# Kernel tuning notes

Measured on AMD Instinct MI355X. Metric: run time of the kernel, lower is better.

Reference implementation:

```python
import jax, jax.numpy as jnp
import numpy as np

B, H, W = 8, 56, 56
DIM, DIM_OUT, NUM_HEADS = 96, 192, 3
Q_STRIDE = (2, 2)


def setup_inputs() -> dict:
    key = jax.random.key(0)
    k1, k2, k3 = jax.random.split(key, 3)
    x = jax.random.normal(k1, (B, H, W, DIM), dtype=jnp.float32)
    W_qkv = jax.random.normal(k2, (DIM, 3 * DIM_OUT), dtype=jnp.float32) * 0.02
    b_qkv = jnp.zeros((3 * DIM_OUT,), dtype=jnp.float32)
    W_proj = jax.random.normal(k3, (DIM_OUT, DIM_OUT), dtype=jnp.float32) * 0.02
    b_proj = jnp.zeros((DIM_OUT,), dtype=jnp.float32)
    return {"x": x, "W_qkv": W_qkv, "b_qkv": b_qkv, "W_proj": W_proj, "b_proj": b_proj}


def reference(x, W_qkv, b_qkv, W_proj, b_proj):
    b, h, w, _ = x.shape
    c = W_proj.shape[0]          # dim_out
    nh = NUM_HEADS
    hd = c // nh                 # head_dim
    sh, sw = Q_STRIDE

    # fused QKV projection: (B,H,W,3*C)
    qkv = jnp.einsum("bhwd,de->bhwe", x, W_qkv) + b_qkv
    qkv = qkv.reshape(b, h * w, 3, nh, hd)
    q, k, v = qkv[:, :, 0], qkv[:, :, 1], qkv[:, :, 2]  # each (B,N,nh,hd)

    # query max-pool over spatial dims (channels = nh*hd, heads interleaved as in original)
    q = q.reshape(b, h, w, c)
    q = q.reshape(b, h // sh, sh, w // sw, sw, c).max(axis=(2, 4))  # (B,H',W',C)
    hn, wn = h // sh, w // sw
    q = q.reshape(b, hn * wn, nh, hd)

    # heads-first layout, scaled q
    q = q.transpose(0, 2, 1, 3) / jnp.sqrt(jnp.asarray(hd, x.dtype))  # (B,nh,Nq,hd)
    k = k.transpose(0, 2, 1, 3)                                       # (B,nh,Nk,hd)
    v = v.transpose(0, 2, 1, 3)

    attn = jax.nn.softmax(jnp.einsum("bnqd,bnkd->bnqk", q, k), axis=-1)
    out = jnp.einsum("bnqk,bnkd->bnqd", attn, v)        # (B,nh,Nq,hd)
    out = out.transpose(0, 2, 1, 3).reshape(b, hn, wn, c)

    return jnp.einsum("bhwc,cd->bhwd", out, W_proj) + b_proj
```

## Files before the change

kernel.cpp:

```cpp
#include <hip/hip_runtime.h>

#define BB    8
#define DIMO  192
#define NH    3
#define HD    64
#define NK    3136
#define NQ    784
#define M1    25088
#define M2    6272
#define KSPLIT 7
#define KSLICE 448
#define PSTR  56

#if __has_builtin(__builtin_amdgcn_mfma_f32_16x16x16bf16_1k)
#define HAVE_MFMA16 1
#else
#define HAVE_MFMA16 0
#endif

typedef __bf16 bf16x8 __attribute__((ext_vector_type(8)));
typedef float f32x4  __attribute__((ext_vector_type(4)));
typedef short s16x4  __attribute__((ext_vector_type(4)));

__device__ inline unsigned short f2bf(float f) {
    unsigned int u = __builtin_bit_cast(unsigned int, f);
    u += 0x7FFFu + ((u >> 16) & 1u);
    return (unsigned short)(u >> 16);
}

__global__ void wprep(const float* __restrict__ Wqkv, const float* __restrict__ Wproj,
                      unsigned short* __restrict__ Wb, unsigned short* __restrict__ Wpb) {
    __shared__ float Ls[192][33];
    const int t = threadIdx.x;
    if (blockIdx.x < 18) {
        const int n0 = blockIdx.x * 32;
        int rr = t >> 5, c = t & 31;
#pragma unroll
        for (int rb = 0; rb < 12; ++rb) {
            int row = rb * 8 + rr;
            Ls[row][c] = Wqkv[(size_t)row * 576 + n0 + c];
        }
        __syncthreads();
        int n = t >> 3, kc = (t & 7) * 12;
#pragma unroll
        for (int j = 0; j < 12; j += 4) {
            ushort4 u = { f2bf(Ls[kc + j][n]), f2bf(Ls[kc + j + 1][n]),
                          f2bf(Ls[kc + j + 2][n]), f2bf(Ls[kc + j + 3][n]) };
            *(ushort4*)(Wb + (size_t)(n0 + n) * 96 + kc + j) = u;
        }
    } else {
        const int n0 = (blockIdx.x - 18) * 32;
        int rr = t >> 5, c = t & 31;
#pragma unroll
        for (int rb = 0; rb < 24; ++rb) {
            int row = rb * 8 + rr;
            Ls[row][c] = Wproj[(size_t)row * 192 + n0 + c];
        }
        __syncthreads();
        int n = t >> 3, kc = (t & 7) * 24;
#pragma unroll
        for (int j = 0; j < 24; j += 4) {
            ushort4 u = { f2bf(Ls[kc + j][n]), f2bf(Ls[kc + j + 1][n]),
                          f2bf(Ls[kc + j + 2][n]), f2bf(Ls[kc + j + 3][n]) };
            *(ushort4*)(Wpb + (size_t)(n0 + n) * 192 + kc + j) = u;
        }
    }
}

__launch_bounds__(256)
__global__ void qkv_fused(const float* __restrict__ x,
                          const unsigned short* __restrict__ Wb,
                          const float* __restrict__ bias,
                          unsigned short* __restrict__ Qpb,
                          unsigned short* __restrict__ Kb,
                          unsigned short* __restrict__ Vt) {
    __shared__ __attribute__((aligned(16))) unsigned short xs[112 * 104];
    const int tid = threadIdx.x;
    const int wave = tid >> 6, lane = tid & 63;
    const int quad = lane >> 4, l16 = lane & 15;
    const int bid = blockIdx.x;

    if (bid < 784) {
        const int sec = (bid < 392) ? 1 : 2;
        const int m0 = ((bid < 392) ? bid : bid - 392) * 64;
#pragma unroll
        for (int i = 0; i < 6; ++i) {
            int f = tid + i * 256;
            int r = f / 24, c4 = f % 24;
            float4 v = ((const float4*)x)[(size_t)(m0 + r) * 24 + c4];
            ushort4 u = { f2bf(v.x), f2bf(v.y), f2bf(v.z), f2bf(v.w) };
            *(ushort4*)&xs[r * 104 + c4 * 4] = u;
        }
        __syncthreads();

        f32x4 acc[12];
#pragma unroll
        for (int i = 0; i < 12; ++i) acc[i] = (f32x4){0.f, 0.f, 0.f, 0.f};

        const unsigned short* wb = Wb + (size_t)(sec * 192 + l16) * 96 + quad * 8;
#pragma unroll
        for (int ch = 0; ch < 3; ++ch) {
            bf16x8 af = *(const bf16x8*)&xs[(wave * 16 + l16) * 104 + ch * 32 + quad * 8];
#pragma unroll
            for (int nf = 0; nf < 12; ++nf) {
                bf16x8 bfr = *(const bf16x8*)(wb + (size_t)nf * 16 * 96 + ch * 32);
                acc[nf] = __builtin_amdgcn_mfma_f32_16x16x32_bf16(af, bfr, acc[nf], 0, 0, 0);
            }
        }

        const int mbase = m0 + wave * 16 + quad * 4;
        if (sec == 1) {
#pragma unroll
            for (int nf = 0; nf < 12; ++nf) {
                int n = nf * 16 + l16;
                float bs = bias[192 + n];
#pragma unroll
                for (int i = 0; i < 4; ++i)
                    Kb[(size_t)(mbase + i) * 192 + n] = f2bf(acc[nf][i] + bs);
            }
        } else {
            int b = m0 / NK;
            int key = mbase - b * NK;
#pragma unroll
            for (int nf = 0; nf < 12; ++nf) {
                int n = nf * 16 + l16;
                float bs = bias[384 + n];
                int hh = n >> 6, dd = n & 63;
                ushort4 u = { f2bf(acc[nf][0] + bs), f2bf(acc[nf][1] + bs),
                              f2bf(acc[nf][2] + bs), f2bf(acc[nf][3] + bs) };
                *(ushort4*)(Vt + ((size_t)((b * 3 + hh) * 64 + dd)) * NK + key) = u;
            }
        }
    } else {
        const int t = bid - 784;
        const int b = t / 28, hq = t % 28;
        const int m0 = b * NK + hq * 112;
#pragma unroll
        for (int i = 0; i < 11; ++i) {
            int f = tid + i * 256;
            if (f < 2688) {
                int r = f / 24, c4 = f % 24;
                float4 v = ((const float4*)x)[(size_t)(m0 + r) * 24 + c4];
                int rp = 2 * (r % 56) + (r / 56);
                ushort4 u = { f2bf(v.x), f2bf(v.y), f2bf(v.z), f2bf(v.w) };
                *(ushort4*)&xs[rp * 104 + c4 * 4] = u;
            }
        }
        __syncthreads();

        f32x4 acc[7][3];
#pragma unroll
        for (int i = 0; i < 7; ++i)
#pragma unroll
            for (int j = 0; j < 3; ++j) acc[i][j] = (f32x4){0.f, 0.f, 0.f, 0.f};

        const unsigned short* wb = Wb + (size_t)(wave * 48 + l16) * 96 + quad * 8;
#pragma unroll
        for (int ch = 0; ch < 3; ++ch) {
            bf16x8 bfr[3];
#pragma unroll
            for (int jf = 0; jf < 3; ++jf)
                bfr[jf] = *(const bf16x8*)(wb + (size_t)jf * 16 * 96 + ch * 32);
#pragma unroll
            for (int mf = 0; mf < 7; ++mf) {
                bf16x8 a = *(const bf16x8*)&xs[(mf * 16 + l16) * 104 + ch * 32 + quad * 8];
#pragma unroll
                for (int jf = 0; jf < 3; ++jf)
                    acc[mf][jf] = __builtin_amdgcn_mfma_f32_16x16x32_bf16(a, bfr[jf], acc[mf][jf], 0, 0, 0);
            }
        }

#pragma unroll
        for (int mf = 0; mf < 7; ++mf) {
            int q = hq * 28 + mf * 4 + quad;
#pragma unroll
            for (int jf = 0; jf < 3; ++jf) {
                int n = wave * 48 + jf * 16 + l16;
                float m = fmaxf(fmaxf(acc[mf][jf][0], acc[mf][jf][1]),
                                fmaxf(acc[mf][jf][2], acc[mf][jf][3]));
                m = (m + bias[n]) * 0.125f;
                int hh = n >> 6, dd = n & 63;
                Qpb[((size_t)(b * 3 + hh) * NQ + q) * 64 + dd] = f2bf(m);
            }
        }
    }
}

__launch_bounds__(256)
__global__ void attn_mfma(const unsigned short* __restrict__ Qpb,
                          const unsigned short* __restrict__ Kb,
                          const unsigned short* __restrict__ Vt,
                          float* __restrict__ Pnum,
                          float* __restrict__ Pden) {
    __shared__ __attribute__((aligned(16))) unsigned short Ks[64 * 88];
    __shared__ __attribute__((aligned(16))) unsigned short Vs[64 * 88];
#if !HAVE_MFMA16
    __shared__ __attribute__((aligned(16))) unsigned short Ps[4 * 32 * PSTR];
#endif

    const int tid = threadIdx.x;
    const int wave = tid >> 6, lane = tid & 63;
    const int quad = lane >> 4, l16 = lane & 15;
    const int bh = blockIdx.y, b = bh / NH, h = bh % NH;
    const int qt = blockIdx.x * 128 + wave * 32;
    const int ks = blockIdx.z, k00 = ks * KSLICE;

    const int srow0 = tid >> 3, sch = (tid & 7) * 8;
    const unsigned short* kg  = Kb + ((size_t)(b * NK + k00) + srow0) * DIMO + h * 64 + sch;
    const unsigned short* kg1 = kg + (size_t)32 * DIMO;
    const unsigned short* vg  = Vt + ((size_t)bh * 64 + srow0) * NK + k00 + sch;
    const unsigned short* vg1 = vg + (size_t)32 * NK;

    uint4 kp0 = *(const uint4*)kg;
    uint4 kp1 = *(const uint4*)kg1;
    uint4 vp0 = *(const uint4*)vg;
    uint4 vp1 = *(const uint4*)vg1;

    int qa = min(qt + l16, NQ - 1);
    int qb = min(qt + 16 + l16, NQ - 1);
    const unsigned short* qpa = Qpb + ((size_t)bh * NQ + qa) * HD + quad * 8;
    const unsigned short* qpc = Qpb + ((size_t)bh * NQ + qb) * HD + quad * 8;
    bf16x8 qf[2][2];
    qf[0][0] = *(const bf16x8*)qpa;  qf[0][1] = *(const bf16x8*)(qpa + 32);
    qf[1][0] = *(const bf16x8*)qpc;  qf[1][1] = *(const bf16x8*)(qpc + 32);

    f32x4 on[4][2];
#pragma unroll
    for (int i = 0; i < 4; ++i)
#pragma unroll
        for (int j = 0; j < 2; ++j) on[i][j] = (f32x4){0.f, 0.f, 0.f, 0.f};
    float dden0 = 0.f, dden1 = 0.f;

#if !HAVE_MFMA16
    unsigned short* myP = Ps + wave * 32 * PSTR;
#endif

    for (int s = 0; s < 7; ++s) {
        __syncthreads();
        *(uint4*)&Ks[srow0 * 88 + sch]        = kp0;
        *(uint4*)&Ks[(srow0 + 32) * 88 + sch] = kp1;
        *(uint4*)&Vs[srow0 * 88 + sch]        = vp0;
        *(uint4*)&Vs[(srow0 + 32) * 88 + sch] = vp1;
        __syncthreads();
        if (s < 6) {
            kp0 = *(const uint4*)(kg  + (size_t)(s + 1) * 64 * DIMO);
            kp1 = *(const uint4*)(kg1 + (size_t)(s + 1) * 64 * DIMO);
            vp0 = *(const uint4*)(vg  + (s + 1) * 64);
            vp1 = *(const uint4*)(vg1 + (s + 1) * 64);
        }

#if HAVE_MFMA16
#pragma unroll
        for (int g = 0; g < 4; ++g) {
            const int krow = (g * 16 + l16) * 88;
            bf16x8 kf0 = *(const bf16x8*)&Ks[krow + quad * 8];
            bf16x8 kf1 = *(const bf16x8*)&Ks[krow + 32 + quad * 8];
            s16x4 vf[4];
#pragma unroll
            for (int dsub = 0; dsub < 4; ++dsub)
                vf[dsub] = *(const s16x4*)&Vs[(dsub * 16 + l16) * 88 + g * 16 + quad * 4];
#pragma unroll
            for (int qsub = 0; qsub < 2; ++qsub) {
                f32x4 sa = (f32x4){0.f, 0.f, 0.f, 0.f};
                sa = __builtin_amdgcn_mfma_f32_16x16x32_bf16(kf0, qf[qsub][0], sa, 0, 0, 0);
                sa = __builtin_amdgcn_mfma_f32_16x16x32_bf16(kf1, qf[qsub][1], sa, 0, 0, 0);
                float p0 = __expf(sa[0]), p1 = __expf(sa[1]);
                float p2 = __expf(sa[2]), p3 = __expf(sa[3]);
                if (qsub == 0) dden0 += (p0 + p1) + (p2 + p3);
                else           dden1 += (p0 + p1) + (p2 + p3);
                s16x4 pb = { (short)f2bf(p0), (short)f2bf(p1),
                             (short)f2bf(p2), (short)f2bf(p3) };
#pragma unroll
                for (int dsub = 0; dsub < 4; ++dsub)
                    on[dsub][qsub] = __builtin_amdgcn_mfma_f32_16x16x16bf16_1k(
                        vf[dsub], pb, on[dsub][qsub], 0, 0, 0);
            }
        }
#else
#pragma unroll
        for (int half = 0; half < 2; ++half) {
#pragma unroll
            for (int ksub = 0; ksub < 2; ++ksub) {
                const int krow = (half * 32 + ksub * 16 + l16) * 88;
                bf16x8 kf0 = *(const bf16x8*)&Ks[krow + quad * 8];
                bf16x8 kf1 = *(const bf16x8*)&Ks[krow + 32 + quad * 8];
#pragma unroll
                for (int qsub = 0; qsub < 2; ++qsub) {
                    f32x4 sa = (f32x4){0.f, 0.f, 0.f, 0.f};
                    sa = __builtin_amdgcn_mfma_f32_16x16x32_bf16(kf0, qf[qsub][0], sa, 0, 0, 0);
                    sa = __builtin_amdgcn_mfma_f32_16x16x32_bf16(kf1, qf[qsub][1], sa, 0, 0, 0);
                    float p0 = __expf(sa[0]), p1 = __expf(sa[1]);
                    float p2 = __expf(sa[2]), p3 = __expf(sa[3]);
                    if (qsub == 0) dden0 += (p0 + p1) + (p2 + p3);
                    else           dden1 += (p0 + p1) + (p2 + p3);
                    ushort4 pw = { f2bf(p0), f2bf(p1), f2bf(p2), f2bf(p3) };
                    *(ushort4*)&myP[(qsub * 16 + l16) * PSTR + ksub * 16 + quad * 4] = pw;
                }
            }
            bf16x8 pf0 = *(const bf16x8*)&myP[l16 * PSTR + quad * 8];
            bf16x8 pf1 = *(const bf16x8*)&myP[(16 + l16) * PSTR + quad * 8];
#pragma unroll
            for (int dsub = 0; dsub < 4; ++dsub) {
                bf16x8 vf = *(const bf16x8*)&Vs[(dsub * 16 + l16) * 88 + half * 32 + quad * 8];
                on[dsub][0] = __builtin_amdgcn_mfma_f32_16x16x32_bf16(vf, pf0, on[dsub][0], 0, 0, 0);
                on[dsub][1] = __builtin_amdgcn_mfma_f32_16x16x32_bf16(vf, pf1, on[dsub][1], 0, 0, 0);
            }
        }
#endif
    }

#pragma unroll
    for (int qsub = 0; qsub < 2; ++qsub) {
        float r = (qsub == 0) ? dden0 : dden1;
        r += __shfl_xor(r, 16, 64);
        r += __shfl_xor(r, 32, 64);
        int q = qt + qsub * 16 + l16;
        if (q < NQ) {
            size_t base = (size_t)ks * (24 * NQ * HD) + ((size_t)bh * NQ + q) * HD + quad * 4;
#pragma unroll
            for (int dsub = 0; dsub < 4; ++dsub)
                *(f32x4*)(Pnum + base + dsub * 16) = on[dsub][qsub];
            if (quad == 0) Pden[ks * (24 * NQ) + bh * NQ + q] = r;
        }
    }
}

__launch_bounds__(256)
__global__ void proj_comb(const float* __restrict__ Pnum,
                          const float* __restrict__ Pden,
                          const unsigned short* __restrict__ Wpb,
                          const float* __restrict__ bproj,
                          float* __restrict__ out) {
    __shared__ __attribute__((aligned(16))) unsigned short as_[16 * 200];
    __shared__ float rden[16][4];
    const int tid = threadIdx.x;
    const int wave = tid >> 6, lane = tid & 63;
    const int quad = lane >> 4, l16 = lane & 15;
    const int m0 = blockIdx.x * 16;

    if (tid < 48) {
        int r = tid / 3, h = tid % 3;
        int gq = m0 + r, b = gq / NQ, qq = gq - b * NQ;
        float den = 0.f;
#pragma unroll
        for (int s = 0; s < KSPLIT; ++s)
            den += Pden[s * (24 * NQ) + (b * 3 + h) * NQ + qq];
        rden[r][h] = 1.0f / den;
    }
    __syncthreads();

    {
        int r = tid >> 4, cl = tid & 15;
        int gq = m0 + r, b = gq / NQ, qq = gq - b * NQ;
#pragma unroll
        for (int i = 0; i < 3; ++i) {
            int c = cl + i * 16;
            int h = c >> 4, d = (c & 15) * 4;
            const float* p = Pnum + ((size_t)(b * 3 + h) * NQ + qq) * 64 + d;
            f32x4 num = (f32x4){0.f, 0.f, 0.f, 0.f};
#pragma unroll
            for (int s = 0; s < KSPLIT; ++s)
                num = num + *(const f32x4*)(p + (size_t)s * (24 * NQ * HD));
            float rc = rden[r][h];
            ushort4 u = { f2bf(num[0] * rc), f2bf(num[1] * rc),
                          f2bf(num[2] * rc), f2bf(num[3] * rc) };
            *(ushort4*)&as_[r * 200 + c * 4] = u;
        }
    }
    __syncthreads();

    f32x4 acc[3];
#pragma unroll
    for (int j = 0; j < 3; ++j) acc[j] = (f32x4){0.f, 0.f, 0.f, 0.f};

    const unsigned short* wp = Wpb + (size_t)(wave * 48 + l16) * 192 + quad * 8;
#pragma unroll
    for (int ch = 0; ch < 6; ++ch) {
        bf16x8 a = *(const bf16x8*)&as_[l16 * 200 + ch * 32 + quad * 8];
#pragma unroll
        for (int jf = 0; jf < 3; ++jf) {
            bf16x8 bfr = *(const bf16x8*)(wp + (size_t)jf * 16 * 192 + ch * 32);
            acc[jf] = __builtin_amdgcn_mfma_f32_16x16x32_bf16(a, bfr, acc[jf], 0, 0, 0);
        }
    }

    const int m = m0 + quad * 4;
#pragma unroll
    for (int jf = 0; jf < 3; ++jf) {
        int n = wave * 48 + jf * 16 + l16;
        float bs = bproj[n];
#pragma unroll
        for (int i = 0; i < 4; ++i)
            out[(size_t)(m + i) * 192 + n] = acc[jf][i] + bs;
    }
}

extern "C" void kernel_launch(void* const* d_in, const int* in_sizes, int n_in,
                              void* d_out, int out_size, void* d_ws, size_t ws_size,
                              hipStream_t stream) {
    const float* x     = (const float*)d_in[0];
    const float* Wqkv  = (const float*)d_in[1];
    const float* bqkv  = (const float*)d_in[2];
    const float* Wproj = (const float*)d_in[3];
    const float* bproj = (const float*)d_in[4];
    float* out = (float*)d_out;

    float* Pnum = (float*)d_ws;
    float* Pden = Pnum + (size_t)KSPLIT * 24 * NQ * HD;
    unsigned short* Qpb = (unsigned short*)(Pden + (size_t)KSPLIT * 24 * NQ);
    unsigned short* Kb  = Qpb + (size_t)24 * NQ * HD;
    unsigned short* Vt  = Kb + (size_t)BB * NK * DIMO;
    unsigned short* Wb  = Vt + (size_t)24 * HD * NK;
    unsigned short* Wpb = Wb + (size_t)576 * 96;

    wprep<<<24, 256, 0, stream>>>(Wqkv, Wproj, Wb, Wpb);

    qkv_fused<<<1008, 256, 0, stream>>>(x, Wb, bqkv, Qpb, Kb, Vt);

    attn_mfma<<<dim3(7, 24, KSPLIT), 256, 0, stream>>>(Qpb, Kb, Vt, Pnum, Pden);

    proj_comb<<<392, 256, 0, stream>>>(Pnum, Pden, Wpb, bproj, out);
}
```

Baseline: 134.3 us.

## Retile attention to 16 queries per wave, fewer key splits, merge K/V projection

The attention kernel now gives each wave 16 queries instead of 32 and splits keys 4 ways (784 keys per slice) instead of 7. The last 64-key step of each slice handles only the 16 leftover keys. This cuts the partial numerator and denominator traffic that proj_comb must combine, and keeps a similar block count. The QKV kernel now computes both K and V from one staged x tile per block, so x is no longer loaded and converted twice. The tail step's prefetch reads past the slice (into neighbouring data or workspace), and the remaining keys are handled with serial per-block loops and fewer registers per wave.

```diff
diff --git a/kernel.cpp b/kernel.cpp
--- a/kernel.cpp
+++ b/kernel.cpp
@@ -8,9 +8,8 @@
 #define NQ    784
 #define M1    25088
 #define M2    6272
-#define KSPLIT 7
-#define KSLICE 448
-#define PSTR  56
+#define KSPLIT 4
+#define KSLICE 784
 
 #if __has_builtin(__builtin_amdgcn_mfma_f32_16x16x16bf16_1k)
 #define HAVE_MFMA16 1
@@ -80,9 +79,8 @@
     const int quad = lane >> 4, l16 = lane & 15;
     const int bid = blockIdx.x;
 
-    if (bid < 784) {
-        const int sec = (bid < 392) ? 1 : 2;
-        const int m0 = ((bid < 392) ? bid : bid - 392) * 64;
+    if (bid < 392) {
+        const int m0 = bid * 64;
 #pragma unroll
         for (int i = 0; i < 6; ++i) {
             int f = tid + i * 256;
@@ -93,46 +91,50 @@
         }
         __syncthreads();
 
-        f32x4 acc[12];
-#pragma unroll
-        for (int i = 0; i < 12; ++i) acc[i] = (f32x4){0.f, 0.f, 0.f, 0.f};
-
-        const unsigned short* wb = Wb + (size_t)(sec * 192 + l16) * 96 + quad * 8;
-#pragma unroll
-        for (int ch = 0; ch < 3; ++ch) {
-            bf16x8 af = *(const bf16x8*)&xs[(wave * 16 + l16) * 104 + ch * 32 + quad * 8];
-#pragma unroll
-            for (int nf = 0; nf < 12; ++nf) {
-                bf16x8 bfr = *(const bf16x8*)(wb + (size_t)nf * 16 * 96 + ch * 32);
-                acc[nf] = __builtin_amdgcn_mfma_f32_16x16x32_bf16(af, bfr, acc[nf], 0, 0, 0);
-            }
-        }
-
         const int mbase = m0 + wave * 16 + quad * 4;
-        if (sec == 1) {
-#pragma unroll
-            for (int nf = 0; nf < 12; ++nf) {
-                int n = nf * 16 + l16;
-                float bs = bias[192 + n];
-#pragma unroll
-                for (int i = 0; i < 4; ++i)
-                    Kb[(size_t)(mbase + i) * 192 + n] = f2bf(acc[nf][i] + bs);
-            }
-        } else {
-            int b = m0 / NK;
-            int key = mbase - b * NK;
-#pragma unroll
-            for (int nf = 0; nf < 12; ++nf) {
-                int n = nf * 16 + l16;
-                float bs = bias[384 + n];
-                int hh = n >> 6, dd = n & 63;
-                ushort4 u = { f2bf(acc[nf][0] + bs), f2bf(acc[nf][1] + bs),
-                              f2bf(acc[nf][2] + bs), f2bf(acc[nf][3] + bs) };
-                *(ushort4*)(Vt + ((size_t)((b * 3 + hh) * 64 + dd)) * NK + key) = u;
+        const int b = m0 / NK;
+        const int key = mbase - b * NK;
+
+#pragma unroll
+        for (int sec = 1; sec <= 2; ++sec) {
+            f32x4 acc[12];
+#pragma unroll
+            for (int i = 0; i < 12; ++i) acc[i] = (f32x4){0.f, 0.f, 0.f, 0.f};
+
+            const unsigned short* wb = Wb + (size_t)(sec * 192 + l16) * 96 + quad * 8;
+#pragma unroll
+            for (int ch = 0; ch < 3; ++ch) {
+                bf16x8 af = *(const bf16x8*)&xs[(wave * 16 + l16) * 104 + ch * 32 + quad * 8];
+#pragma unroll
+                for (int nf = 0; nf < 12; ++nf) {
+                    bf16x8 bfr = *(const bf16x8*)(wb + (size_t)nf * 16 * 96 + ch * 32);
+                    acc[nf] = __builtin_amdgcn_mfma_f32_16x16x32_bf16(af, bfr, acc[nf], 0, 0, 0);
+                }
+            }
+
+            if (sec == 1) {
+#pragma unroll
+                for (int nf = 0; nf < 12; ++nf) {
+                    int n = nf * 16 + l16;
+                    float bs = bias[192 + n];
+#pragma unroll
+                    for (int i = 0; i < 4; ++i)
+                        Kb[(size_t)(mbase + i) * 192 + n] = f2bf(acc[nf][i] + bs);
+                }
+            } else {
+#pragma unroll
+                for (int nf = 0; nf < 12; ++nf) {
+                    int n = nf * 16 + l16;
+                    float bs = bias[384 + n];
+                    int hh = n >> 6, dd = n & 63;
+                    ushort4 u = { f2bf(acc[nf][0] + bs), f2bf(acc[nf][1] + bs),
+                                  f2bf(acc[nf][2] + bs), f2bf(acc[nf][3] + bs) };
+                    *(ushort4*)(Vt + ((size_t)((b * 3 + hh) * 64 + dd)) * NK + key) = u;
+                }
             }
         }
     } else {
-        const int t = bid - 784;
+        const int t = bid - 392;
         const int b = t / 28, hq = t % 28;
         const int m0 = b * NK + hq * 112;
 #pragma unroll
@@ -195,14 +197,14 @@
     __shared__ __attribute__((aligned(16))) unsigned short Ks[64 * 88];
     __shared__ __attribute__((aligned(16))) unsigned short Vs[64 * 88];
 #if !HAVE_MFMA16
-    __shared__ __attribute__((aligned(16))) unsigned short Ps[4 * 32 * PSTR];
+    __shared__ __attribute__((aligned(16))) unsigned short Ps[4 * 16 * 72];
 #endif
 
     const int tid = threadIdx.x;
     const int wave = tid >> 6, lane = tid & 63;
     const int quad = lane >> 4, l16 = lane & 15;
     const int bh = blockIdx.y, b = bh / NH, h = bh % NH;
-    const int qt = blockIdx.x * 128 + wave * 32;
+    const int qt = blockIdx.x * 64 + wave * 16;
     const int ks = blockIdx.z, k00 = ks * KSLICE;
 
     const int srow0 = tid >> 3, sch = (tid & 7) * 8;
@@ -216,112 +218,84 @@
     uint4 vp0 = *(const uint4*)vg;
     uint4 vp1 = *(const uint4*)vg1;
 
-    int qa = min(qt + l16, NQ - 1);
-    int qb = min(qt + 16 + l16, NQ - 1);
-    const unsigned short* qpa = Qpb + ((size_t)bh * NQ + qa) * HD + quad * 8;
-    const unsigned short* qpc = Qpb + ((size_t)bh * NQ + qb) * HD + quad * 8;
-    bf16x8 qf[2][2];
-    qf[0][0] = *(const bf16x8*)qpa;  qf[0][1] = *(const bf16x8*)(qpa + 32);
-    qf[1][0] = *(const bf16x8*)qpc;  qf[1][1] = *(const bf16x8*)(qpc + 32);
-
-    f32x4 on[4][2];
-#pragma unroll
-    for (int i = 0; i < 4; ++i)
-#pragma unroll
-        for (int j = 0; j < 2; ++j) on[i][j] = (f32x4){0.f, 0.f, 0.f, 0.f};
-    float dden0 = 0.f, dden1 = 0.f;
+    int qv = min(qt + l16, NQ - 1);
+    const unsigned short* qp = Qpb + ((size_t)bh * NQ + qv) * HD + quad * 8;
+    bf16x8 qf0 = *(const bf16x8*)qp;
+    bf16x8 qf1 = *(const bf16x8*)(qp + 32);
+
+    f32x4 on[4];
+#pragma unroll
+    for (int i = 0; i < 4; ++i) on[i] = (f32x4){0.f, 0.f, 0.f, 0.f};
+    float dden = 0.f;
 
 #if !HAVE_MFMA16
-    unsigned short* myP = Ps + wave * 32 * PSTR;
-#endif
-
-    for (int s = 0; s < 7; ++s) {
+    unsigned short* myP = Ps + wave * 16 * 72;
+#endif
+
+    for (int s = 0; s < 13; ++s) {
         __syncthreads();
         *(uint4*)&Ks[srow0 * 88 + sch]        = kp0;
         *(uint4*)&Ks[(srow0 + 32) * 88 + sch] = kp1;
         *(uint4*)&Vs[srow0 * 88 + sch]        = vp0;
         *(uint4*)&Vs[(srow0 + 32) * 88 + sch] = vp1;
         __syncthreads();
-        if (s < 6) {
+        if (s < 12) {
             kp0 = *(const uint4*)(kg  + (size_t)(s + 1) * 64 * DIMO);
             kp1 = *(const uint4*)(kg1 + (size_t)(s + 1) * 64 * DIMO);
             vp0 = *(const uint4*)(vg  + (s + 1) * 64);
             vp1 = *(const uint4*)(vg1 + (s + 1) * 64);
         }
 
-#if HAVE_MFMA16
-#pragma unroll
-        for (int g = 0; g < 4; ++g) {
+        const int ng = (s == 12) ? 1 : 4;
+        for (int g = 0; g < ng; ++g) {
             const int krow = (g * 16 + l16) * 88;
             bf16x8 kf0 = *(const bf16x8*)&Ks[krow + quad * 8];
             bf16x8 kf1 = *(const bf16x8*)&Ks[krow + 32 + quad * 8];
-            s16x4 vf[4];
-#pragma unroll
-            for (int dsub = 0; dsub < 4; ++dsub)
-                vf[dsub] = *(const s16x4*)&Vs[(dsub * 16 + l16) * 88 + g * 16 + quad * 4];
-#pragma unroll
-            for (int qsub = 0; qsub < 2; ++qsub) {
-                f32x4 sa = (f32x4){0.f, 0.f, 0.f, 0.f};
-                sa = __builtin_amdgcn_mfma_f32_16x16x32_bf16(kf0, qf[qsub][0], sa, 0, 0, 0);
-                sa = __builtin_amdgcn_mfma_f32_16x16x32_bf16(kf1, qf[qsub][1], sa, 0, 0, 0);
-                float p0 = __expf(sa[0]), p1 = __expf(sa[1]);
-                float p2 = __expf(sa[2]), p3 = __expf(sa[3]);
-                if (qsub == 0) dden0 += (p0 + p1) + (p2 + p3);
-                else           dden1 += (p0 + p1) + (p2 + p3);
-                s16x4 pb = { (short)f2bf(p0), (short)f2bf(p1),
-                             (short)f2bf(p2), (short)f2bf(p3) };
-#pragma unroll
-                for (int dsub = 0; dsub < 4; ++dsub)
-                    on[dsub][qsub] = __builtin_amdgcn_mfma_f32_16x16x16bf16_1k(
-                        vf[dsub], pb, on[dsub][qsub], 0, 0, 0);
-            }
-        }
+            f32x4 sa = (f32x4){0.f, 0.f, 0.f, 0.f};
+            sa = __builtin_amdgcn_mfma_f32_16x16x32_bf16(kf0, qf0, sa, 0, 0, 0);
+            sa = __builtin_amdgcn_mfma_f32_16x16x32_bf16(kf1, qf1, sa, 0, 0, 0);
+            float p0 = __expf(sa[0]), p1 = __expf(sa[1]);
+            float p2 = __expf(sa[2]), p3 = __expf(sa[3]);
+            dden += (p0 + p1) + (p2 + p3);
+#if HAVE_MFMA16
+            s16x4 pb = { (short)f2bf(p0), (short)f2bf(p1),
+                         (short)f2bf(p2), (short)f2bf(p3) };
+#pragma unroll
+            for (int dsub = 0; dsub < 4; ++dsub) {
+                s16x4 vf = *(const s16x4*)&Vs[(dsub * 16 + l16) * 88 + g * 16 + quad * 4];
+                on[dsub] = __builtin_amdgcn_mfma_f32_16x16x16bf16_1k(vf, pb, on[dsub], 0, 0, 0);
+            }
 #else
-#pragma unroll
-        for (int half = 0; half < 2; ++half) {
-#pragma unroll
-            for (int ksub = 0; ksub < 2; ++ksub) {
-                const int krow = (half * 32 + ksub * 16 + l16) * 88;
-                bf16x8 kf0 = *(const bf16x8*)&Ks[krow + quad * 8];
-                bf16x8 kf1 = *(const bf16x8*)&Ks[krow + 32 + quad * 8];
-#pragma unroll
-                for (int qsub = 0; qsub < 2; ++qsub) {
-                    f32x4 sa = (f32x4){0.f, 0.f, 0.f, 0.f};
-                    sa = __builtin_amdgcn_mfma_f32_16x16x32_bf16(kf0, qf[qsub][0], sa, 0, 0, 0);
-                    sa = __builtin_amdgcn_mfma_f32_16x16x32_bf16(kf1, qf[qsub][1], sa, 0, 0, 0);
-                    float p0 = __expf(sa[0]), p1 = __expf(sa[1]);
-                    float p2 = __expf(sa[2]), p3 = __expf(sa[3]);
-                    if (qsub == 0) dden0 += (p0 + p1) + (p2 + p3);
-                    else           dden1 += (p0 + p1) + (p2 + p3);
-                    ushort4 pw = { f2bf(p0), f2bf(p1), f2bf(p2), f2bf(p3) };
-                    *(ushort4*)&myP[(qsub * 16 + l16) * PSTR + ksub * 16 + quad * 4] = pw;
-                }
-            }
-            bf16x8 pf0 = *(const bf16x8*)&myP[l16 * PSTR + quad * 8];
-            bf16x8 pf1 = *(const bf16x8*)&myP[(16 + l16) * PSTR + quad * 8];
+            ushort4 pw = { f2bf(p0), f2bf(p1), f2bf(p2), f2bf(p3) };
+            *(ushort4*)&myP[l16 * 72 + g * 16 + quad * 4] = pw;
+#endif
+        }
+#if !HAVE_MFMA16
+        if (s == 12) {
+            ushort4 z = { 0, 0, 0, 0 };
+            *(ushort4*)&myP[l16 * 72 + 16 + quad * 4] = z;
+        }
+        const int nhalf = (s == 12) ? 1 : 2;
+        for (int half = 0; half < nhalf; ++half) {
+            bf16x8 pf = *(const bf16x8*)&myP[l16 * 72 + half * 32 + quad * 8];
 #pragma unroll
             for (int dsub = 0; dsub < 4; ++dsub) {
                 bf16x8 vf = *(const bf16x8*)&Vs[(dsub * 16 + l16) * 88 + half * 32 + quad * 8];
-                on[dsub][0] = __builtin_amdgcn_mfma_f32_16x16x32_bf16(vf, pf0, on[dsub][0], 0, 0, 0);
-                on[dsub][1] = __builtin_amdgcn_mfma_f32_16x16x32_bf16(vf, pf1, on[dsub][1], 0, 0, 0);
-            }
-        }
-#endif
-    }
-
-#pragma unroll
-    for (int qsub = 0; qsub < 2; ++qsub) {
-        float r = (qsub == 0) ? dden0 : dden1;
-        r += __shfl_xor(r, 16, 64);
-        r += __shfl_xor(r, 32, 64);
-        int q = qt + qsub * 16 + l16;
-        if (q < NQ) {
-            size_t base = (size_t)ks * (24 * NQ * HD) + ((size_t)bh * NQ + q) * HD + quad * 4;
-#pragma unroll
-            for (int dsub = 0; dsub < 4; ++dsub)
-                *(f32x4*)(Pnum + base + dsub * 16) = on[dsub][qsub];
-            if (quad == 0) Pden[ks * (24 * NQ) + bh * NQ + q] = r;
-        }
+                on[dsub] = __builtin_amdgcn_mfma_f32_16x16x32_bf16(vf, pf, on[dsub], 0, 0, 0);
+            }
+        }
+#endif
+    }
+
+    dden += __shfl_xor(dden, 16, 64);
+    dden += __shfl_xor(dden, 32, 64);
+    int q = qt + l16;
+    if (q < NQ) {
+        size_t base = (size_t)ks * (24 * NQ * HD) + ((size_t)bh * NQ + q) * HD + quad * 4;
+#pragma unroll
+        for (int dsub = 0; dsub < 4; ++dsub)
+            *(f32x4*)(Pnum + base + dsub * 16) = on[dsub];
+        if (quad == 0) Pden[ks * (24 * NQ) + bh * NQ + q] = dden;
     }
 }
 
@@ -415,9 +389,9 @@
 
     wprep<<<24, 256, 0, stream>>>(Wqkv, Wproj, Wb, Wpb);
 
-    qkv_fused<<<1008, 256, 0, stream>>>(x, Wb, bqkv, Qpb, Kb, Vt);
-
-    attn_mfma<<<dim3(7, 24, KSPLIT), 256, 0, stream>>>(Qpb, Kb, Vt, Pnum, Pden);
+    qkv_fused<<<616, 256, 0, stream>>>(x, Wb, bqkv, Qpb, Kb, Vt);
+
+    attn_mfma<<<dim3(13, 24, KSPLIT), 256, 0, stream>>>(Qpb, Kb, Vt, Pnum, Pden);
 
     proj_comb<<<392, 256, 0, stream>>>(Pnum, Pden, Wpb, bproj, out);
 }
```

Result: slower. 140.9 us (+4.9%).

## Merge K/V projection blocks, use exp2 with folded scale, MFMA row sums

Applied to the files above, without the earlier changes.

The QKV kernel now computes both the K and V sections in one block from a single staged bf16 copy of x, rather than launching separate blocks that each reload and convert x. The query scale now includes log2(e), so attention can use the hardware exp2 instead of __expf. Probabilities are packed to bf16 with a cheaper round-half-up perm sequence. Softmax denominators are accumulated with an extra MFMA against a ones vector instead of scalar adds and cross-lane shuffles. The trade-off is more MFMA work per tile, a slightly different bf16 rounding, and higher register use in the merged K/V blocks.

```diff
diff --git a/kernel.cpp b/kernel.cpp
--- a/kernel.cpp
+++ b/kernel.cpp
@@ -12,12 +12,20 @@
 #define KSLICE 448
 #define PSTR  56
 
+#define QSCALE 0.18033688011112042f
+
 #if __has_builtin(__builtin_amdgcn_mfma_f32_16x16x16bf16_1k)
 #define HAVE_MFMA16 1
 #else
 #define HAVE_MFMA16 0
 #endif
 
+#if __has_builtin(__builtin_amdgcn_exp2f)
+#define FEXP2(x) __builtin_amdgcn_exp2f(x)
+#else
+#define FEXP2(x) exp2f(x)
+#endif
+
 typedef __bf16 bf16x8 __attribute__((ext_vector_type(8)));
 typedef float f32x4  __attribute__((ext_vector_type(4)));
 typedef short s16x4  __attribute__((ext_vector_type(4)));
@@ -26,6 +34,12 @@
     unsigned int u = __builtin_bit_cast(unsigned int, f);
     u += 0x7FFFu + ((u >> 16) & 1u);
     return (unsigned short)(u >> 16);
+}
+
+__device__ inline unsigned int pk_bf16(float a, float b) {
+    unsigned int ua = __builtin_bit_cast(unsigned int, a) + 0x8000u;
+    unsigned int ub = __builtin_bit_cast(unsigned int, b) + 0x8000u;
+    return __builtin_amdgcn_perm(ub, ua, 0x07060302u);
 }
 
 __global__ void wprep(const float* __restrict__ Wqkv, const float* __restrict__ Wproj,
@@ -80,9 +94,8 @@
     const int quad = lane >> 4, l16 = lane & 15;
     const int bid = blockIdx.x;
 
-    if (bid < 784) {
-        const int sec = (bid < 392) ? 1 : 2;
-        const int m0 = ((bid < 392) ? bid : bid - 392) * 64;
+    if (bid < 392) {
+        const int m0 = bid * 64;
 #pragma unroll
         for (int i = 0; i < 6; ++i) {
             int f = tid + i * 256;
@@ -93,46 +106,50 @@
         }
         __syncthreads();
 
-        f32x4 acc[12];
-#pragma unroll
-        for (int i = 0; i < 12; ++i) acc[i] = (f32x4){0.f, 0.f, 0.f, 0.f};
-
-        const unsigned short* wb = Wb + (size_t)(sec * 192 + l16) * 96 + quad * 8;
-#pragma unroll
-        for (int ch = 0; ch < 3; ++ch) {
-            bf16x8 af = *(const bf16x8*)&xs[(wave * 16 + l16) * 104 + ch * 32 + quad * 8];
-#pragma unroll
-            for (int nf = 0; nf < 12; ++nf) {
-                bf16x8 bfr = *(const bf16x8*)(wb + (size_t)nf * 16 * 96 + ch * 32);
-                acc[nf] = __builtin_amdgcn_mfma_f32_16x16x32_bf16(af, bfr, acc[nf], 0, 0, 0);
-            }
-        }
-
         const int mbase = m0 + wave * 16 + quad * 4;
-        if (sec == 1) {
-#pragma unroll
-            for (int nf = 0; nf < 12; ++nf) {
-                int n = nf * 16 + l16;
-                float bs = bias[192 + n];
-#pragma unroll
-                for (int i = 0; i < 4; ++i)
-                    Kb[(size_t)(mbase + i) * 192 + n] = f2bf(acc[nf][i] + bs);
-            }
-        } else {
-            int b = m0 / NK;
-            int key = mbase - b * NK;
-#pragma unroll
-            for (int nf = 0; nf < 12; ++nf) {
-                int n = nf * 16 + l16;
-                float bs = bias[384 + n];
-                int hh = n >> 6, dd = n & 63;
-                ushort4 u = { f2bf(acc[nf][0] + bs), f2bf(acc[nf][1] + bs),
-                              f2bf(acc[nf][2] + bs), f2bf(acc[nf][3] + bs) };
-                *(ushort4*)(Vt + ((size_t)((b * 3 + hh) * 64 + dd)) * NK + key) = u;
+        const int b = m0 / NK;
+        const int key = mbase - b * NK;
+
+#pragma unroll
+        for (int sec = 1; sec <= 2; ++sec) {
+            f32x4 acc[12];
+#pragma unroll
+            for (int i = 0; i < 12; ++i) acc[i] = (f32x4){0.f, 0.f, 0.f, 0.f};
+
+            const unsigned short* wb = Wb + (size_t)(sec * 192 + l16) * 96 + quad * 8;
+#pragma unroll
+            for (int ch = 0; ch < 3; ++ch) {
+                bf16x8 af = *(const bf16x8*)&xs[(wave * 16 + l16) * 104 + ch * 32 + quad * 8];
+#pragma unroll
+                for (int nf = 0; nf < 12; ++nf) {
+                    bf16x8 bfr = *(const bf16x8*)(wb + (size_t)nf * 16 * 96 + ch * 32);
+                    acc[nf] = __builtin_amdgcn_mfma_f32_16x16x32_bf16(af, bfr, acc[nf], 0, 0, 0);
+                }
+            }
+
+            if (sec == 1) {
+#pragma unroll
+                for (int nf = 0; nf < 12; ++nf) {
+                    int n = nf * 16 + l16;
+                    float bs = bias[192 + n];
+#pragma unroll
+                    for (int i = 0; i < 4; ++i)
+                        Kb[(size_t)(mbase + i) * 192 + n] = f2bf(acc[nf][i] + bs);
+                }
+            } else {
+#pragma unroll
+                for (int nf = 0; nf < 12; ++nf) {
+                    int n = nf * 16 + l16;
+                    float bs = bias[384 + n];
+                    int hh = n >> 6, dd = n & 63;
+                    ushort4 u = { f2bf(acc[nf][0] + bs), f2bf(acc[nf][1] + bs),
+                                  f2bf(acc[nf][2] + bs), f2bf(acc[nf][3] + bs) };
+                    *(ushort4*)(Vt + ((size_t)((b * 3 + hh) * 64 + dd)) * NK + key) = u;
+                }
             }
         }
     } else {
-        const int t = bid - 784;
+        const int t = bid - 392;
         const int b = t / 28, hq = t % 28;
         const int m0 = b * NK + hq * 112;
 #pragma unroll
@@ -178,7 +195,7 @@
                 int n = wave * 48 + jf * 16 + l16;
                 float m = fmaxf(fmaxf(acc[mf][jf][0], acc[mf][jf][1]),
                                 fmaxf(acc[mf][jf][2], acc[mf][jf][3]));
-                m = (m + bias[n]) * 0.125f;
+                m = (m + bias[n]) * QSCALE;
                 int hh = n >> 6, dd = n & 63;
                 Qpb[((size_t)(b * 3 + hh) * NQ + q) * 64 + dd] = f2bf(m);
             }
@@ -229,9 +246,16 @@
     for (int i = 0; i < 4; ++i)
 #pragma unroll
         for (int j = 0; j < 2; ++j) on[i][j] = (f32x4){0.f, 0.f, 0.f, 0.f};
-    float dden0 = 0.f, dden1 = 0.f;
-
-#if !HAVE_MFMA16
+    f32x4 dn[2];
+    dn[0] = (f32x4){0.f, 0.f, 0.f, 0.f};
+    dn[1] = (f32x4){0.f, 0.f, 0.f, 0.f};
+
+#if HAVE_MFMA16
+    const short one16 = (short)0x3F80;
+    s16x4 ones4 = { one16, one16, one16, one16 };
+#else
+    const __bf16 one = (__bf16)1.0f;
+    bf16x8 ones8 = { one, one, one, one, one, one, one, one };
     unsigned short* myP = Ps + wave * 32 * PSTR;
 #endif
 
@@ -264,12 +288,11 @@
                 f32x4 sa = (f32x4){0.f, 0.f, 0.f, 0.f};
                 sa = __builtin_amdgcn_mfma_f32_16x16x32_bf16(kf0, qf[qsub][0], sa, 0, 0, 0);
                 sa = __builtin_amdgcn_mfma_f32_16x16x32_bf16(kf1, qf[qsub][1], sa, 0, 0, 0);
-                float p0 = __expf(sa[0]), p1 = __expf(sa[1]);
-                float p2 = __expf(sa[2]), p3 = __expf(sa[3]);
-                if (qsub == 0) dden0 += (p0 + p1) + (p2 + p3);
-                else           dden1 += (p0 + p1) + (p2 + p3);
-                s16x4 pb = { (short)f2bf(p0), (short)f2bf(p1),
-                             (short)f2bf(p2), (short)f2bf(p3) };
+                float p0 = FEXP2(sa[0]), p1 = FEXP2(sa[1]);
+                float p2 = FEXP2(sa[2]), p3 = FEXP2(sa[3]);
+                uint2 pk = { pk_bf16(p0, p1), pk_bf16(p2, p3) };
+                s16x4 pb = __builtin_bit_cast(s16x4, pk);
+                dn[qsub] = __builtin_amdgcn_mfma_f32_16x16x16bf16_1k(ones4, pb, dn[qsub], 0, 0, 0);
 #pragma unroll
                 for (int dsub = 0; dsub < 4; ++dsub)
                     on[dsub][qsub] = __builtin_amdgcn_mfma_f32_16x16x16bf16_1k(
@@ -289,16 +312,16 @@
                     f32x4 sa = (f32x4){0.f, 0.f, 0.f, 0.f};
                     sa = __builtin_amdgcn_mfma_f32_16x16x32_bf16(kf0, qf[qsub][0], sa, 0, 0, 0);
                     sa = __builtin_amdgcn_mfma_f32_16x16x32_bf16(kf1, qf[qsub][1], sa, 0, 0, 0);
-                    float p0 = __expf(sa[0]), p1 = __expf(sa[1]);
-                    float p2 = __expf(sa[2]), p3 = __expf(sa[3]);
-                    if (qsub == 0) dden0 += (p0 + p1) + (p2 + p3);
-                    else           dden1 += (p0 + p1) + (p2 + p3);
-                    ushort4 pw = { f2bf(p0), f2bf(p1), f2bf(p2), f2bf(p3) };
-                    *(ushort4*)&myP[(qsub * 16 + l16) * PSTR + ksub * 16 + quad * 4] = pw;
+                    float p0 = FEXP2(sa[0]), p1 = FEXP2(sa[1]);
+                    float p2 = FEXP2(sa[2]), p3 = FEXP2(sa[3]);
+                    uint2 pk = { pk_bf16(p0, p1), pk_bf16(p2, p3) };
+                    *(uint2*)&myP[(qsub * 16 + l16) * PSTR + ksub * 16 + quad * 4] = pk;
                 }
             }
             bf16x8 pf0 = *(const bf16x8*)&myP[l16 * PSTR + quad * 8];
             bf16x8 pf1 = *(const bf16x8*)&myP[(16 + l16) * PSTR + quad * 8];
+            dn[0] = __builtin_amdgcn_mfma_f32_16x16x32_bf16(ones8, pf0, dn[0], 0, 0, 0);
+            dn[1] = __builtin_amdgcn_mfma_f32_16x16x32_bf16(ones8, pf1, dn[1], 0, 0, 0);
 #pragma unroll
             for (int dsub = 0; dsub < 4; ++dsub) {
                 bf16x8 vf = *(const bf16x8*)&Vs[(dsub * 16 + l16) * 88 + half * 32 + quad * 8];
@@ -311,16 +334,13 @@
 
 #pragma unroll
     for (int qsub = 0; qsub < 2; ++qsub) {
-        float r = (qsub == 0) ? dden0 : dden1;
-        r += __shfl_xor(r, 16, 64);
-        r += __shfl_xor(r, 32, 64);
         int q = qt + qsub * 16 + l16;
         if (q < NQ) {
             size_t base = (size_t)ks * (24 * NQ * HD) + ((size_t)bh * NQ + q) * HD + quad * 4;
 #pragma unroll
             for (int dsub = 0; dsub < 4; ++dsub)
                 *(f32x4*)(Pnum + base + dsub * 16) = on[dsub][qsub];
-            if (quad == 0) Pden[ks * (24 * NQ) + bh * NQ + q] = r;
+            if (quad == 0) Pden[ks * (24 * NQ) + bh * NQ + q] = dn[qsub][0];
         }
     }
 }
@@ -415,7 +435,7 @@
 
     wprep<<<24, 256, 0, stream>>>(Wqkv, Wproj, Wb, Wpb);
 
-    qkv_fused<<<1008, 256, 0, stream>>>(x, Wb, bqkv, Qpb, Kb, Vt);
+    qkv_fused<<<616, 256, 0, stream>>>(x, Wb, bqkv, Qpb, Kb, Vt);
 
     attn_mfma<<<dim3(7, 24, KSPLIT), 256, 0, stream>>>(Qpb, Kb, Vt, Pnum, Pden);
 
```

New measurement: 138.4 us. +3.1%, slower.
